# Optimization experiments

Measured on AMD Instinct MI355X. Metric: run time of the kernel, lower is better.

## Reference

```python
import jax, jax.numpy as jnp
import numpy as np

B, N, K = 32, 4096, 8          # batch, num input features (64x64 map), num slots
HID, D, DM = 256, 256, 512     # hid_dim, slot_dim, mlp_hid_dim
ITERS = 3
TEMP = 1.0
EPS = 1e-8
SCALE = D ** -0.5              # (slot_dim // num_heads) ** -0.5, heads=1


def layer_norm(x, g, b):
    m = jnp.mean(x, axis=-1, keepdims=True)
    v = jnp.mean((x - m) ** 2, axis=-1, keepdims=True)
    return (x - m) * jax.lax.rsqrt(v + 1e-5) * g + b


def setup_inputs() -> dict:
    key = jax.random.key(0)
    ks = jax.random.split(key, 20)
    s = 0.02
    inp = {
        "inputs": jax.random.normal(ks[0], (B, N, HID), jnp.float32),
        "noise": jax.random.normal(ks[1], (B, K, D), jnp.float32),
        "slots_mu": jax.random.normal(ks[2], (1, 1, D), jnp.float32),
        "slots_sigma": jnp.abs(jax.random.normal(ks[3], (1, 1, D), jnp.float32)),
        "ln_in_g": jnp.ones((HID,), jnp.float32),
        "ln_in_b": jnp.zeros((HID,), jnp.float32),
        "ln_slots_g": jnp.ones((D,), jnp.float32),
        "ln_slots_b": jnp.zeros((D,), jnp.float32),
        "ln_mlp_g": jnp.ones((D,), jnp.float32),
        "ln_mlp_b": jnp.zeros((D,), jnp.float32),
        # Linear weights stored [in, out]
        "Wq": jax.random.normal(ks[4], (D, D), jnp.float32) * s,
        "bq": jnp.zeros((D,), jnp.float32),
        "Wk": jax.random.normal(ks[5], (HID, D), jnp.float32) * s,
        "bk": jnp.zeros((D,), jnp.float32),
        "Wv": jax.random.normal(ks[6], (HID, D), jnp.float32) * s,
        "bv": jnp.zeros((D,), jnp.float32),
        # GRUCell params (torch layout transposed to [in, 3D])
        "W_ih": jax.random.normal(ks[7], (D, 3 * D), jnp.float32) * s,
        "W_hh": jax.random.normal(ks[8], (D, 3 * D), jnp.float32) * s,
        "b_ih": jnp.zeros((3 * D,), jnp.float32),
        "b_hh": jnp.zeros((3 * D,), jnp.float32),
        # residual MLP
        "W1": jax.random.normal(ks[9], (D, DM), jnp.float32) * s,
        "b1": jnp.zeros((DM,), jnp.float32),
        "W2": jax.random.normal(ks[10], (DM, D), jnp.float32) * s,
        "b2": jnp.zeros((D,), jnp.float32),
    }
    return inp


def reference(inputs, noise, slots_mu, slots_sigma,
              ln_in_g, ln_in_b, ln_slots_g, ln_slots_b, ln_mlp_g, ln_mlp_b,
              Wq, bq, Wk, bk, Wv, bv,
              W_ih, W_hh, b_ih, b_hh,
              W1, b1, W2, b2):
    x = layer_norm(inputs, ln_in_g, ln_in_b)            # [B,N,HID]
    k = x @ Wk + bk                                     # [B,N,D]
    v = x @ Wv + bv                                     # [B,N,D]

    slots = slots_mu + slots_sigma * noise              # [B,K,D]

    for _ in range(ITERS):
        slots_prev = slots
        s = layer_norm(slots, ln_slots_g, ln_slots_b)
        q = s @ Wq + bq                                  # [B,K,D]
        dots = jnp.einsum('bkd,bnd->bkn', q, k) * SCALE / TEMP
        attn = jax.nn.softmax(dots, axis=1)              # inverted: over slot axis
        attn = attn + EPS
        attn = attn / jnp.sum(attn, axis=2, keepdims=True)  # weighted mean over keys
        updates = jnp.einsum('bkn,bnd->bkd', attn, v)    # [B,K,D]

        # GRUCell on flattened (B*K, D)
        xg = updates.reshape(-1, D)
        h = slots_prev.reshape(-1, D)
        gi = xg @ W_ih + b_ih
        gh = h @ W_hh + b_hh
        i_r, i_z, i_n = jnp.split(gi, 3, axis=-1)
        h_r, h_z, h_n = jnp.split(gh, 3, axis=-1)
        r = jax.nn.sigmoid(i_r + h_r)
        z = jax.nn.sigmoid(i_z + h_z)
        n = jnp.tanh(i_n + r * h_n)
        h = (1.0 - z) * n + z * h
        slots = h.reshape(B, K, D)

        # residual MLP
        m = layer_norm(slots, ln_mlp_g, ln_mlp_b)
        slots = slots + (jax.nn.relu(m @ W1 + b1) @ W2 + b2)

    return slots
```

## Files before the change

### kernel.cpp

```cpp
#include <hip/hip_runtime.h>
#include <hip/hip_bf16.h>

#define NB 32
#define NPOS 4096
#define NSLOT 8
#define HIDD 256
#define DDIM 256
#define SCALE_F 0.0625f
#define EPS_F 1e-8f
#define NCHUNK 32
#define CPOS 128
#define TPOS 32

typedef __attribute__((ext_vector_type(4))) float f32x4;
typedef __attribute__((ext_vector_type(8))) short s16x8;
typedef __attribute__((ext_vector_type(2))) unsigned int u32x2;

__device__ __forceinline__ unsigned short f2bf(float f) {
    unsigned int x = __float_as_uint(f);
    x = (x + 0x7fffu + ((x >> 16) & 1u)) >> 16;
    return (unsigned short)x;
}
__device__ __forceinline__ float bf_lo(unsigned u) { return __uint_as_float(u << 16); }
__device__ __forceinline__ float bf_hi(unsigned u) { return __uint_as_float(u & 0xffff0000u); }

__global__ __launch_bounds__(256) void k_ln_in(
        const float* __restrict__ x, const float* __restrict__ g,
        const float* __restrict__ b, unsigned short* __restrict__ lnx) {
    int lane = threadIdx.x & 63;
    int wave = threadIdx.x >> 6;
    long row = (long)blockIdx.x * 4 + wave;
    const float4* xr = (const float4*)(x + row * 256);
    float4 v = xr[lane];
    float s = v.x + v.y + v.z + v.w;
    float sq = v.x * v.x + v.y * v.y + v.z * v.z + v.w * v.w;
    #pragma unroll
    for (int m = 32; m; m >>= 1) { s += __shfl_xor(s, m); sq += __shfl_xor(sq, m); }
    float mean = s * 0.00390625f;
    float rstd = rsqrtf(sq * 0.00390625f - mean * mean + 1e-5f);
    const float4 gg = ((const float4*)g)[lane];
    const float4 bb = ((const float4*)b)[lane];
    ushort4 o;
    o.x = f2bf((v.x - mean) * rstd * gg.x + bb.x);
    o.y = f2bf((v.y - mean) * rstd * gg.y + bb.y);
    o.z = f2bf((v.z - mean) * rstd * gg.z + bb.z);
    o.w = f2bf((v.w - mean) * rstd * gg.w + bb.w);
    ((ushort4*)(lnx + row * 256))[lane] = o;
}

__device__ __forceinline__ unsigned packrow(const float* __restrict__ W, int hp, int N, int c) {
    return (unsigned)f2bf(W[(2*hp)*N + c]) | ((unsigned)f2bf(W[(2*hp+1)*N + c]) << 16);
}

__global__ __launch_bounds__(256) void k_prep(
        const float* __restrict__ Wq, const float* __restrict__ Wk,
        const float* __restrict__ Wv, const float* __restrict__ Wih,
        const float* __restrict__ Whh, const float* __restrict__ W1,
        const float* __restrict__ W2,
        unsigned* __restrict__ WqP, unsigned* __restrict__ WkTP,
        unsigned* __restrict__ WvP, unsigned* __restrict__ WihP,
        unsigned* __restrict__ WhhP, unsigned* __restrict__ W1P,
        unsigned* __restrict__ W2P) {
    int i = blockIdx.x * 256 + threadIdx.x;
    if (i < 32768) {
        int hp = i >> 8, c = i & 255;
        WqP[i] = packrow(Wq, hp, 256, c);
        WvP[i] = packrow(Wv, hp, 256, c);
        WkTP[i] = (unsigned)f2bf(Wk[c*256 + 2*hp]) | ((unsigned)f2bf(Wk[c*256 + 2*hp + 1]) << 16);
    }
    if (i < 65536) {
        int hp1 = i >> 9, c1 = i & 511;
        W1P[i] = packrow(W1, hp1, 512, c1);
        int hp2 = i >> 8, c2 = i & 255;
        W2P[i] = packrow(W2, hp2, 256, c2);
    }
    if (i < 98304) {
        int hp = i / 768, c = i % 768;
        WihP[i] = packrow(Wih, hp, 768, c);
        WhhP[i] = packrow(Whh, hp, 768, c);
    }
}

__device__ __forceinline__ void qk_tail(
        float v0, float v1, int b, int s0,
        const float* __restrict__ lng, const float* __restrict__ lnb,
        const float* __restrict__ Wq, const float* __restrict__ bq,
        const float* __restrict__ Wk, const float* __restrict__ bk,
        unsigned short* __restrict__ qkg, float* __restrict__ qbkg,
        float (*sh)[256], float (*red)[4]) {
    int c = threadIdx.x;
    float s_0 = v0, q_0 = v0 * v0, s_1 = v1, q_1 = v1 * v1;
    #pragma unroll
    for (int m = 32; m; m >>= 1) {
        s_0 += __shfl_xor(s_0, m); q_0 += __shfl_xor(q_0, m);
        s_1 += __shfl_xor(s_1, m); q_1 += __shfl_xor(q_1, m);
    }
    if ((c & 63) == 0) { int w = c >> 6; red[w][0]=s_0; red[w][1]=q_0; red[w][2]=s_1; red[w][3]=q_1; }
    __syncthreads();
    float S0 = red[0][0]+red[1][0]+red[2][0]+red[3][0];
    float Q0 = red[0][1]+red[1][1]+red[2][1]+red[3][1];
    float S1 = red[0][2]+red[1][2]+red[2][2]+red[3][2];
    float Q1 = red[0][3]+red[1][3]+red[2][3]+red[3][3];
    float m0 = S0 * 0.00390625f, r0 = rsqrtf(Q0 * 0.00390625f - m0*m0 + 1e-5f);
    float m1 = S1 * 0.00390625f, r1 = rsqrtf(Q1 * 0.00390625f - m1*m1 + 1e-5f);
    float gc = lng[c], bc = lnb[c];
    sh[0][c] = (v0 - m0) * r0 * gc + bc;
    sh[1][c] = (v1 - m1) * r1 * gc + bc;
    __syncthreads();
    float qa0 = bq[c], qa1 = qa0;
    for (int h = 0; h < 256; h += 4) {
        float w0 = Wq[(h+0)*256+c], w1 = Wq[(h+1)*256+c];
        float w2 = Wq[(h+2)*256+c], w3 = Wq[(h+3)*256+c];
        float4 x0 = *(const float4*)&sh[0][h], x1 = *(const float4*)&sh[1][h];
        qa0 += x0.x*w0 + x0.y*w1 + x0.z*w2 + x0.w*w3;
        qa1 += x1.x*w0 + x1.y*w1 + x1.z*w2 + x1.w*w3;
    }
    __syncthreads();
    sh[0][c] = qa0; sh[1][c] = qa1;
    float bkc = bk[c];
    float p0 = qa0 * bkc, p1 = qa1 * bkc;
    #pragma unroll
    for (int m = 32; m; m >>= 1) { p0 += __shfl_xor(p0, m); p1 += __shfl_xor(p1, m); }
    __syncthreads();
    if ((c & 63) == 0) { int w = c >> 6; red[w][0] = p0; red[w][1] = p1; }
    __syncthreads();
    if (c < 2) qbkg[b*8 + s0 + c] = SCALE_F * (red[0][c]+red[1][c]+red[2][c]+red[3][c]);
    float k0 = 0.f, k1 = 0.f;
    const float* wkr = Wk + (long)c * 256;
    for (int d = 0; d < 256; d += 4) {
        float4 wk4 = *(const float4*)&wkr[d];
        float4 x0 = *(const float4*)&sh[0][d], x1 = *(const float4*)&sh[1][d];
        k0 += x0.x*wk4.x + x0.y*wk4.y + x0.z*wk4.z + x0.w*wk4.w;
        k1 += x1.x*wk4.x + x1.y*wk4.y + x1.z*wk4.z + x1.w*wk4.w;
    }
    qkg[(b*8 + s0    )*256 + c] = f2bf(SCALE_F * k0);
    qkg[(b*8 + s0 + 1)*256 + c] = f2bf(SCALE_F * k1);
}

__global__ __launch_bounds__(256) void k_init(
        const float* __restrict__ noise, const float* __restrict__ mu,
        const float* __restrict__ sig, const float* __restrict__ lng,
        const float* __restrict__ lnb, const float* __restrict__ Wq,
        const float* __restrict__ bq, const float* __restrict__ Wk,
        const float* __restrict__ bk, float* __restrict__ slots,
        unsigned short* __restrict__ qkg, float* __restrict__ qbkg) {
    __shared__ float sh[2][256];
    __shared__ float red[4][4];
    int b = blockIdx.x >> 2, rp = blockIdx.x & 3;
    int s0 = rp * 2, r0 = b * 8 + s0;
    int c = threadIdx.x;
    float v0 = mu[c] + sig[c] * noise[r0*256 + c];
    float v1 = mu[c] + sig[c] * noise[(r0+1)*256 + c];
    slots[r0*256 + c] = v0;
    slots[(r0+1)*256 + c] = v1;
    qk_tail(v0, v1, b, s0, lng, lnb, Wq, bq, Wk, bk, qkg, qbkg, sh, red);
}

__global__ __launch_bounds__(128) void k_stream(
        const unsigned short* __restrict__ lnx, const unsigned short* __restrict__ qk,
        const float* __restrict__ qbk, float* __restrict__ Upart,
        float* __restrict__ dpart) {
    __shared__ unsigned short xt[TPOS * 256];
    __shared__ float Ured[8 * 256];
    __shared__ float dred[8];
    int b = blockIdx.x >> 5, ch = blockIdx.x & 31;
    int t = threadIdx.x;
    int l = t & 63, w = t >> 6;
    for (int i = t; i < 2048; i += 128) Ured[i] = 0.f;
    if (t < 8) dred[t] = 0.f;
    int slot = l & 15, g = l >> 4;
    s16x8 qkf[8];
    float qbkv = 0.f;
    if (slot < 8) {
        const unsigned short* qrow = qk + (b*8 + slot) * 256;
        #pragma unroll
        for (int hk = 0; hk < 8; hk++)
            qkf[hk] = *(const s16x8*)(qrow + hk*32 + 8*g);
        qbkv = qbk[b*8 + slot];
    } else {
        #pragma unroll
        for (int hk = 0; hk < 8; hk++) qkf[hk] = (s16x8)0;
    }
    f32x4 uacc[16];
    #pragma unroll
    for (int i = 0; i < 16; i++) uacc[i] = (f32x4)0.f;
    float dreg = 0.f;
    int gbase = (b * NPOS + ch * CPOS) * 256;
    int pw = w * 16;
    __syncthreads();
    for (int tile = 0; tile < 4; tile++) {
        #pragma unroll
        for (int i = 0; i < 8; i++) {
            int c = t + 128 * i;
            int p = c >> 5, hc = c & 31;
            int4 v = *(const int4*)(lnx + gbase + (tile*TPOS + p)*256 + hc*8);
            *(int4*)&xt[p*256 + ((hc ^ (p & 15)) << 3)] = v;
        }
        __syncthreads();
        f32x4 acc = (f32x4)0.f;
        {
            int prow = pw + (l & 15);
            const unsigned short* xrow = &xt[prow * 256];
            int sw = prow & 15;
            #pragma unroll
            for (int hk = 0; hk < 8; hk++) {
                s16x8 a = *(const s16x8*)(xrow + (((hk*4 + g) ^ sw) << 3));
                acc = __builtin_amdgcn_mfma_f32_16x16x32_bf16(a, qkf[hk], acc, 0, 0, 0);
            }
        }
        float at[4];
        #pragma unroll
        for (int r = 0; r < 4; r++) {
            float v = acc[r] + qbkv;
            float m = v;
            m = fmaxf(m, __shfl_xor(m, 1));
            m = fmaxf(m, __shfl_xor(m, 2));
            m = fmaxf(m, __shfl_xor(m, 4));
            float e = __expf(v - m);
            float sum = e;
            sum += __shfl_xor(sum, 1);
            sum += __shfl_xor(sum, 2);
            sum += __shfl_xor(sum, 4);
            float a = e / sum;
            at[r] = a;
            dreg += a;
        }
        u32x2 a2;
        a2.x = (unsigned)f2bf(at[0]) | ((unsigned)f2bf(at[1]) << 16);
        a2.y = (unsigned)f2bf(at[2]) | ((unsigned)f2bf(at[3]) << 16);
        int p0 = pw + 4 * g;
        int hl = l & 7;
        #pragma unroll
        for (int hc = 0; hc < 16; hc++) {
            int hcol = hc * 2 + ((l & 15) >> 3);
            unsigned e0 = xt[(p0+0)*256 + ((hcol ^ ((p0+0) & 15)) << 3) + hl];
            unsigned e1 = xt[(p0+1)*256 + ((hcol ^ ((p0+1) & 15)) << 3) + hl];
            unsigned e2 = xt[(p0+2)*256 + ((hcol ^ ((p0+2) & 15)) << 3) + hl];
            unsigned e3 = xt[(p0+3)*256 + ((hcol ^ ((p0+3) & 15)) << 3) + hl];
            u32x2 b2;
            b2.x = e0 | (e1 << 16);
            b2.y = e2 | (e3 << 16);
            asm volatile("v_mfma_f32_16x16x16_bf16 %0, %1, %2, %0"
                         : "+v"(uacc[hc]) : "v"(a2), "v"(b2));
        }
        __syncthreads();
    }
    if (g < 2) {
        #pragma unroll
        for (int hc = 0; hc < 16; hc++) {
            int h = hc * 16 + (l & 15);
            #pragma unroll
            for (int r = 0; r < 4; r++)
                atomicAdd(&Ured[(4*g + r)*256 + h], uacc[hc][r]);
        }
    }
    dreg += __shfl_xor(dreg, 16);
    dreg += __shfl_xor(dreg, 32);
    if (slot < 8 && g == 0) atomicAdd(&dred[slot], dreg);
    __syncthreads();
    float* up = Upart + (long)(b * NCHUNK + ch) * 2048;
    for (int i = t; i < 2048; i += 128) up[i] = Ured[i];
    if (t < 8) dpart[(b * NCHUNK + ch) * 8 + t] = dred[t];
}

__device__ __forceinline__ float ln1024(float v, int c, const float* __restrict__ g,
                                        const float* __restrict__ b, float (*red)[2]) {
    float s1 = v, s2 = v * v;
    #pragma unroll
    for (int m = 32; m; m >>= 1) { s1 += __shfl_xor(s1, m); s2 += __shfl_xor(s2, m); }
    int w = threadIdx.x >> 6;
    if ((threadIdx.x & 63) == 0) { red[w][0] = s1; red[w][1] = s2; }
    __syncthreads();
    float S = 0.f, Q = 0.f;
    #pragma unroll
    for (int i = 0; i < 16; i++) { S += red[i][0]; Q += red[i][1]; }
    float mean = S * (1.f/1024.f);
    float rstd = rsqrtf(Q * (1.f/1024.f) - mean*mean + 1e-5f);
    __syncthreads();
    return (v - mean) * rstd * g[c] + b[c];
}

__global__ __launch_bounds__(1024) void k_post(
        const float* __restrict__ Upart, const float* __restrict__ dpart,
        const unsigned* __restrict__ WvP, const float* __restrict__ bv,
        const unsigned* __restrict__ WihP, const unsigned* __restrict__ WhhP,
        const float* __restrict__ bih, const float* __restrict__ bhh,
        const float* __restrict__ lnmg, const float* __restrict__ lnmb,
        const unsigned* __restrict__ W1P, const float* __restrict__ b1,
        const unsigned* __restrict__ W2P, const float* __restrict__ b2,
        const float* __restrict__ lnsg, const float* __restrict__ lnsb,
        const unsigned* __restrict__ WqP, const float* __restrict__ bq,
        const unsigned* __restrict__ WkTP, const float* __restrict__ bk,
        float* __restrict__ slots, unsigned short* __restrict__ qkg,
        float* __restrict__ qbkg, float* __restrict__ outp, int last) {
    __shared__ float A[256];
    __shared__ float B[256];
    __shared__ float P4[4][256];
    __shared__ float G[12][256];
    __shared__ float H2[2][512];
    __shared__ float H[512];
    __shared__ float red[16][2];
    __shared__ float scal[1];
    int r = blockIdx.x, b = r >> 3, s = r & 7;
    int t = threadIdx.x, c = t & 255, q = t >> 8;
    {
        float u = 0.f;
        const float* ub = Upart + (long)b * NCHUNK * 2048 + s * 256 + c;
        #pragma unroll
        for (int i = 0; i < 8; i++) u += ub[(q * 8 + i) * 2048];
        P4[q][c] = u;
        if (q == 1) B[c] = slots[r * 256 + c];
        if (t < 32) {
            float dv = dpart[(b * NCHUNK + t) * 8 + s];
            #pragma unroll
            for (int m = 16; m; m >>= 1) dv += __shfl_xor(dv, m);
            if (t == 0) scal[0] = dv;
        }
    }
    __syncthreads();
    float dn = 1.f / (scal[0] + (float)NPOS * EPS_F);
    if (q == 0) A[c] = P4[0][c] + P4[1][c] + P4[2][c] + P4[3][c];
    __syncthreads();
    {
        float acc = 0.f;
        const unsigned* wp = WvP + q * 32 * 256 + c;
        const float* ap = A + q * 64;
        #pragma unroll 8
        for (int i = 0; i < 32; i++) {
            unsigned wv = wp[i * 256];
            acc += ap[2*i] * bf_lo(wv) + ap[2*i+1] * bf_hi(wv);
        }
        P4[q][c] = acc;
    }
    __syncthreads();
    float updc = (P4[0][c] + P4[1][c] + P4[2][c] + P4[3][c]) * dn + bv[c];
    if (q == 0) A[c] = updc;
    __syncthreads();
    {
        const float* src = (q < 2) ? A : B;
        const unsigned* W = (q < 2) ? WihP : WhhP;
        int base = (q & 1) * 64;
        float ar = 0.f, az = 0.f, an = 0.f;
        #pragma unroll 4
        for (int i = 0; i < 64; i++) {
            int hp = base + i;
            float a0 = src[2*hp], a1 = src[2*hp+1];
            unsigned w0 = W[hp*768 + c];
            unsigned w1 = W[hp*768 + c + 256];
            unsigned w2 = W[hp*768 + c + 512];
            ar += a0*bf_lo(w0) + a1*bf_hi(w0);
            az += a0*bf_lo(w1) + a1*bf_hi(w1);
            an += a0*bf_lo(w2) + a1*bf_hi(w2);
        }
        G[q*3+0][c] = ar; G[q*3+1][c] = az; G[q*3+2][c] = an;
    }
    __syncthreads();
    float spc = B[c];
    float gir = bih[c]     + G[0][c] + G[3][c];
    float giz = bih[c+256] + G[1][c] + G[4][c];
    float gin = bih[c+512] + G[2][c] + G[5][c];
    float ghr = bhh[c]     + G[6][c] + G[9][c];
    float ghz = bhh[c+256] + G[7][c] + G[10][c];
    float ghn = bhh[c+512] + G[8][c] + G[11][c];
    float rg = 1.f/(1.f + __expf(-(gir+ghr)));
    float zg = 1.f/(1.f + __expf(-(giz+ghz)));
    float ng = tanhf(gin + rg*ghn);
    float hnew = (1.f - zg)*ng + zg*spc;
    float mmc = ln1024(hnew, c, lnmg, lnmb, red);
    if (q == 0) A[c] = mmc;
    __syncthreads();
    {
        int j = t & 511, kh = t >> 9;
        float acc = 0.f;
        #pragma unroll 8
        for (int i = 0; i < 64; i++) {
            int hp = kh*64 + i;
            unsigned wv = W1P[hp*512 + j];
            acc += A[2*hp]*bf_lo(wv) + A[2*hp+1]*bf_hi(wv);
        }
        H2[kh][j] = acc;
    }
    __syncthreads();
    if (t < 512) H[t] = fmaxf(H2[0][t] + H2[1][t] + b1[t], 0.f);
    __syncthreads();
    {
        float acc = 0.f;
        const unsigned* wp = W2P + q * 64 * 256 + c;
        const float* hb = H + q * 128;
        #pragma unroll 8
        for (int i = 0; i < 64; i++) {
            unsigned wv = wp[i * 256];
            acc += hb[2*i]*bf_lo(wv) + hb[2*i+1]*bf_hi(wv);
        }
        P4[q][c] = acc;
    }
    __syncthreads();
    float outc = hnew + P4[0][c] + P4[1][c] + P4[2][c] + P4[3][c] + b2[c];
    if (t < 256) {
        slots[r*256 + c] = outc;
        if (last) outp[r*256 + c] = outc;
    }
    if (last) return;
    float sc = ln1024(outc, c, lnsg, lnsb, red);
    if (q == 0) A[c] = sc;
    __syncthreads();
    {
        float acc = 0.f;
        const unsigned* wp = WqP + q * 32 * 256 + c;
        const float* ap = A + q * 64;
        #pragma unroll 8
        for (int i = 0; i < 32; i++) {
            unsigned wv = wp[i * 256];
            acc += ap[2*i]*bf_lo(wv) + ap[2*i+1]*bf_hi(wv);
        }
        P4[q][c] = acc;
    }
    __syncthreads();
    float qc = P4[0][c] + P4[1][c] + P4[2][c] + P4[3][c] + bq[c];
    {
        float v = qc * bk[c];
        #pragma unroll
        for (int m = 32; m; m >>= 1) v += __shfl_xor(v, m);
        int w = t >> 6;
        if ((t & 63) == 0) red[w][0] = v;
        __syncthreads();
        if (t == 0) {
            float S = 0.f;
            #pragma unroll
            for (int i = 0; i < 16; i++) S += red[i][0];
            qbkg[r] = SCALE_F * 0.25f * S;
        }
    }
    if (q == 0) A[c] = qc;
    __syncthreads();
    {
        float acc = 0.f;
        const unsigned* wp = WkTP + q * 32 * 256 + c;
        const float* ap = A + q * 64;
        #pragma unroll 8
        for (int i = 0; i < 32; i++) {
            unsigned wv = wp[i * 256];
            acc += ap[2*i]*bf_lo(wv) + ap[2*i+1]*bf_hi(wv);
        }
        P4[q][c] = acc;
    }
    __syncthreads();
    if (t < 256) qkg[r*256 + c] = f2bf(SCALE_F * (P4[0][c] + P4[1][c] + P4[2][c] + P4[3][c]));
}

extern "C" void kernel_launch(void* const* d_in, const int* in_sizes, int n_in,
                              void* d_out, int out_size, void* d_ws, size_t ws_size,
                              hipStream_t stream) {
    const float* inputs = (const float*)d_in[0];
    const float* noise  = (const float*)d_in[1];
    const float* mu     = (const float*)d_in[2];
    const float* sig    = (const float*)d_in[3];
    const float* lnig   = (const float*)d_in[4];
    const float* lnib   = (const float*)d_in[5];
    const float* lnsg   = (const float*)d_in[6];
    const float* lnsb   = (const float*)d_in[7];
    const float* lnmg   = (const float*)d_in[8];
    const float* lnmb   = (const float*)d_in[9];
    const float* Wq     = (const float*)d_in[10];
    const float* bq     = (const float*)d_in[11];
    const float* Wk     = (const float*)d_in[12];
    const float* bk     = (const float*)d_in[13];
    const float* Wv     = (const float*)d_in[14];
    const float* bv     = (const float*)d_in[15];
    const float* Wih    = (const float*)d_in[16];
    const float* Whh    = (const float*)d_in[17];
    const float* bih    = (const float*)d_in[18];
    const float* bhh    = (const float*)d_in[19];
    const float* W1     = (const float*)d_in[20];
    const float* b1     = (const float*)d_in[21];
    const float* W2     = (const float*)d_in[22];
    const float* b2     = (const float*)d_in[23];

    char* ws = (char*)d_ws;
    unsigned short* lnx = (unsigned short*)ws;
    size_t off = (size_t)NB * NPOS * HIDD * 2;
    unsigned short* qkb = (unsigned short*)(ws + off); off += (size_t)NB*NSLOT*HIDD*2;
    float* qbk   = (float*)(ws + off); off += (size_t)NB*NSLOT*4;
    float* Upart = (float*)(ws + off); off += (size_t)NB*NCHUNK*NSLOT*HIDD*4;
    float* dpart = (float*)(ws + off); off += (size_t)NB*NCHUNK*NSLOT*4;
    float* slots = (float*)(ws + off); off += (size_t)NB*NSLOT*DDIM*4;
    unsigned* WqP  = (unsigned*)(ws + off); off += 32768u*4;
    unsigned* WkTP = (unsigned*)(ws + off); off += 32768u*4;
    unsigned* WvP  = (unsigned*)(ws + off); off += 32768u*4;
    unsigned* WihP = (unsigned*)(ws + off); off += 98304u*4;
    unsigned* WhhP = (unsigned*)(ws + off); off += 98304u*4;
    unsigned* W1P  = (unsigned*)(ws + off); off += 65536u*4;
    unsigned* W2P  = (unsigned*)(ws + off); off += 65536u*4;

    k_prep<<<384, 256, 0, stream>>>(Wq, Wk, Wv, Wih, Whh, W1, W2,
                                    WqP, WkTP, WvP, WihP, WhhP, W1P, W2P);
    k_ln_in<<<NB*NPOS/4, 256, 0, stream>>>(inputs, lnig, lnib, lnx);
    k_init<<<NB*4, 256, 0, stream>>>(noise, mu, sig, lnsg, lnsb, Wq, bq, Wk, bk,
                                     slots, qkb, qbk);
    for (int it = 0; it < 3; it++) {
        k_stream<<<NB*NCHUNK, 128, 0, stream>>>(lnx, qkb, qbk, Upart, dpart);
        k_post<<<NB*NSLOT, 1024, 0, stream>>>(Upart, dpart,
                                              WvP, bv, WihP, WhhP, bih, bhh,
                                              lnmg, lnmb, W1P, b1, W2P, b2,
                                              lnsg, lnsb, WqP, bq, WkTP, bk,
                                              slots, qkb, qbk, (float*)d_out,
                                              it == 2 ? 1 : 0);
    }
}
```

Baseline: 242.9 us.

## Split post-processing into per-batch kernels, precompute Wq·Wkᵀ, use fp16 dot2

The monolithic per-slot k_post kernel is replaced by a chain of smaller kernels: reduce, value projection, GRU, two MLP stages, and a query/key kernel. Each of these processes all 8 slots of a batch, so every weight load is reused across 8 rows. The query and key projections are folded algebraically into one precomputed matrix M1 = Wq·Wkᵀ plus bias vectors, which removes one GEMV per iteration. Packed weights move from bf16 to fp16 and use the hardware fdot2 instruction. The cost is about six extra kernel launches per iteration, extra global round-trips for intermediates, and a change in the rounding of the precomputed fused matrix and of fp16 activations.

```diff
diff --git a/kernel.cpp b/kernel.cpp
--- a/kernel.cpp
+++ b/kernel.cpp
@@ -15,14 +15,54 @@
 typedef __attribute__((ext_vector_type(4))) float f32x4;
 typedef __attribute__((ext_vector_type(8))) short s16x8;
 typedef __attribute__((ext_vector_type(2))) unsigned int u32x2;
+typedef _Float16 h16x2 __attribute__((ext_vector_type(2)));
 
 __device__ __forceinline__ unsigned short f2bf(float f) {
     unsigned int x = __float_as_uint(f);
     x = (x + 0x7fffu + ((x >> 16) & 1u)) >> 16;
     return (unsigned short)x;
 }
-__device__ __forceinline__ float bf_lo(unsigned u) { return __uint_as_float(u << 16); }
-__device__ __forceinline__ float bf_hi(unsigned u) { return __uint_as_float(u & 0xffff0000u); }
+__device__ __forceinline__ unsigned short f2h(float f) {
+    _Float16 h = (_Float16)f;
+    return __builtin_bit_cast(unsigned short, h);
+}
+__device__ __forceinline__ h16x2 u2h(unsigned u) { return __builtin_bit_cast(h16x2, u); }
+__device__ __forceinline__ h16x2 mkh(float a0, float a1) {
+    h16x2 r; r[0] = (_Float16)a0; r[1] = (_Float16)a1; return r;
+}
+
+__device__ __forceinline__ float blkred(float v, float* red4) {
+    #pragma unroll
+    for (int m = 32; m; m >>= 1) v += __shfl_xor(v, m);
+    int w = threadIdx.x >> 6;
+    if ((threadIdx.x & 63) == 0) red4[w] = v;
+    __syncthreads();
+    float s = red4[0] + red4[1] + red4[2] + red4[3];
+    __syncthreads();
+    return s;
+}
+
+__device__ __forceinline__ void ln8rows(float (*sl)[256], const float* __restrict__ g,
+                                        const float* __restrict__ b) {
+    int lane = threadIdx.x & 63, wv = threadIdx.x >> 6;
+    #pragma unroll
+    for (int rr = 0; rr < 2; rr++) {
+        int s = wv * 2 + rr;
+        float ss = 0.f, sq = 0.f;
+        #pragma unroll
+        for (int j = 0; j < 4; j++) { float v = sl[s][lane*4+j]; ss += v; sq += v*v; }
+        #pragma unroll
+        for (int m = 32; m; m >>= 1) { ss += __shfl_xor(ss, m); sq += __shfl_xor(sq, m); }
+        float mean = ss * 0.00390625f;
+        float rstd = rsqrtf(sq * 0.00390625f - mean*mean + 1e-5f);
+        #pragma unroll
+        for (int j = 0; j < 4; j++) {
+            int d = lane*4 + j;
+            sl[s][d] = (sl[s][d] - mean) * rstd * g[d] + b[d];
+        }
+    }
+    __syncthreads();
+}
 
 __global__ __launch_bounds__(256) void k_ln_in(
         const float* __restrict__ x, const float* __restrict__ g,
@@ -48,112 +88,102 @@
     ((ushort4*)(lnx + row * 256))[lane] = o;
 }
 
-__device__ __forceinline__ unsigned packrow(const float* __restrict__ W, int hp, int N, int c) {
-    return (unsigned)f2bf(W[(2*hp)*N + c]) | ((unsigned)f2bf(W[(2*hp+1)*N + c]) << 16);
+__device__ __forceinline__ unsigned packrowh(const float* __restrict__ W, int hp, int N, int c) {
+    return (unsigned)f2h(W[(2*hp)*N + c]) | ((unsigned)f2h(W[(2*hp+1)*N + c]) << 16);
 }
 
 __global__ __launch_bounds__(256) void k_prep(
-        const float* __restrict__ Wq, const float* __restrict__ Wk,
         const float* __restrict__ Wv, const float* __restrict__ Wih,
         const float* __restrict__ Whh, const float* __restrict__ W1,
         const float* __restrict__ W2,
-        unsigned* __restrict__ WqP, unsigned* __restrict__ WkTP,
         unsigned* __restrict__ WvP, unsigned* __restrict__ WihP,
         unsigned* __restrict__ WhhP, unsigned* __restrict__ W1P,
         unsigned* __restrict__ W2P) {
     int i = blockIdx.x * 256 + threadIdx.x;
     if (i < 32768) {
         int hp = i >> 8, c = i & 255;
-        WqP[i] = packrow(Wq, hp, 256, c);
-        WvP[i] = packrow(Wv, hp, 256, c);
-        WkTP[i] = (unsigned)f2bf(Wk[c*256 + 2*hp]) | ((unsigned)f2bf(Wk[c*256 + 2*hp + 1]) << 16);
+        WvP[i] = packrowh(Wv, hp, 256, c);
     }
     if (i < 65536) {
         int hp1 = i >> 9, c1 = i & 511;
-        W1P[i] = packrow(W1, hp1, 512, c1);
+        W1P[i] = packrowh(W1, hp1, 512, c1);
         int hp2 = i >> 8, c2 = i & 255;
-        W2P[i] = packrow(W2, hp2, 256, c2);
+        W2P[i] = packrowh(W2, hp2, 256, c2);
     }
     if (i < 98304) {
         int hp = i / 768, c = i % 768;
-        WihP[i] = packrow(Wih, hp, 768, c);
-        WhhP[i] = packrow(Whh, hp, 768, c);
-    }
-}
-
-__device__ __forceinline__ void qk_tail(
-        float v0, float v1, int b, int s0,
-        const float* __restrict__ lng, const float* __restrict__ lnb,
-        const float* __restrict__ Wq, const float* __restrict__ bq,
-        const float* __restrict__ Wk, const float* __restrict__ bk,
-        unsigned short* __restrict__ qkg, float* __restrict__ qbkg,
-        float (*sh)[256], float (*red)[4]) {
-    int c = threadIdx.x;
-    float s_0 = v0, q_0 = v0 * v0, s_1 = v1, q_1 = v1 * v1;
-    #pragma unroll
-    for (int m = 32; m; m >>= 1) {
-        s_0 += __shfl_xor(s_0, m); q_0 += __shfl_xor(q_0, m);
-        s_1 += __shfl_xor(s_1, m); q_1 += __shfl_xor(q_1, m);
-    }
-    if ((c & 63) == 0) { int w = c >> 6; red[w][0]=s_0; red[w][1]=q_0; red[w][2]=s_1; red[w][3]=q_1; }
-    __syncthreads();
-    float S0 = red[0][0]+red[1][0]+red[2][0]+red[3][0];
-    float Q0 = red[0][1]+red[1][1]+red[2][1]+red[3][1];
-    float S1 = red[0][2]+red[1][2]+red[2][2]+red[3][2];
-    float Q1 = red[0][3]+red[1][3]+red[2][3]+red[3][3];
-    float m0 = S0 * 0.00390625f, r0 = rsqrtf(Q0 * 0.00390625f - m0*m0 + 1e-5f);
-    float m1 = S1 * 0.00390625f, r1 = rsqrtf(Q1 * 0.00390625f - m1*m1 + 1e-5f);
-    float gc = lng[c], bc = lnb[c];
-    sh[0][c] = (v0 - m0) * r0 * gc + bc;
-    sh[1][c] = (v1 - m1) * r1 * gc + bc;
-    __syncthreads();
-    float qa0 = bq[c], qa1 = qa0;
-    for (int h = 0; h < 256; h += 4) {
-        float w0 = Wq[(h+0)*256+c], w1 = Wq[(h+1)*256+c];
-        float w2 = Wq[(h+2)*256+c], w3 = Wq[(h+3)*256+c];
-        float4 x0 = *(const float4*)&sh[0][h], x1 = *(const float4*)&sh[1][h];
-        qa0 += x0.x*w0 + x0.y*w1 + x0.z*w2 + x0.w*w3;
-        qa1 += x1.x*w0 + x1.y*w1 + x1.z*w2 + x1.w*w3;
-    }
-    __syncthreads();
-    sh[0][c] = qa0; sh[1][c] = qa1;
-    float bkc = bk[c];
-    float p0 = qa0 * bkc, p1 = qa1 * bkc;
-    #pragma unroll
-    for (int m = 32; m; m >>= 1) { p0 += __shfl_xor(p0, m); p1 += __shfl_xor(p1, m); }
-    __syncthreads();
-    if ((c & 63) == 0) { int w = c >> 6; red[w][0] = p0; red[w][1] = p1; }
-    __syncthreads();
-    if (c < 2) qbkg[b*8 + s0 + c] = SCALE_F * (red[0][c]+red[1][c]+red[2][c]+red[3][c]);
-    float k0 = 0.f, k1 = 0.f;
-    const float* wkr = Wk + (long)c * 256;
-    for (int d = 0; d < 256; d += 4) {
-        float4 wk4 = *(const float4*)&wkr[d];
-        float4 x0 = *(const float4*)&sh[0][d], x1 = *(const float4*)&sh[1][d];
-        k0 += x0.x*wk4.x + x0.y*wk4.y + x0.z*wk4.z + x0.w*wk4.w;
-        k1 += x1.x*wk4.x + x1.y*wk4.y + x1.z*wk4.z + x1.w*wk4.w;
-    }
-    qkg[(b*8 + s0    )*256 + c] = f2bf(SCALE_F * k0);
-    qkg[(b*8 + s0 + 1)*256 + c] = f2bf(SCALE_F * k1);
-}
-
-__global__ __launch_bounds__(256) void k_init(
+        WihP[i] = packrowh(Wih, hp, 768, c);
+        WhhP[i] = packrowh(Whh, hp, 768, c);
+    }
+}
+
+__global__ __launch_bounds__(256) void k_fuse(
+        const float* __restrict__ Wq, const float* __restrict__ Wk,
+        const float* __restrict__ bq, const float* __restrict__ bk,
+        float* __restrict__ M1, float* __restrict__ v1,
+        float* __restrict__ w2, float* __restrict__ sc2) {
+    __shared__ float wq[256], bqL[256];
+    __shared__ float red4[4];
+    int e = blockIdx.x, t = threadIdx.x;
+    wq[t] = Wq[e*256 + t];
+    bqL[t] = bq[t];
+    __syncthreads();
+    const float4* wkr = (const float4*)(Wk + (long)t * 256);
+    float acc = 0.f;
+    for (int d = 0; d < 64; d++) {
+        float4 k4 = wkr[d];
+        acc += wq[4*d]*k4.x + wq[4*d+1]*k4.y + wq[4*d+2]*k4.z + wq[4*d+3]*k4.w;
+    }
+    M1[e*256 + t] = acc;
+    float p = blkred(wq[t] * bk[t], red4);
+    if (t == 0) w2[e] = p;
+    if (e == 0) {
+        float a2 = 0.f;
+        for (int d = 0; d < 64; d++) {
+            float4 k4 = wkr[d];
+            a2 += bqL[4*d]*k4.x + bqL[4*d+1]*k4.y + bqL[4*d+2]*k4.z + bqL[4*d+3]*k4.w;
+        }
+        v1[t] = a2;
+        float p2 = blkred(bqL[t] * bk[t], red4);
+        if (t == 0) sc2[0] = p2;
+    }
+}
+
+__global__ __launch_bounds__(256) void k_init2(
         const float* __restrict__ noise, const float* __restrict__ mu,
-        const float* __restrict__ sig, const float* __restrict__ lng,
-        const float* __restrict__ lnb, const float* __restrict__ Wq,
-        const float* __restrict__ bq, const float* __restrict__ Wk,
-        const float* __restrict__ bk, float* __restrict__ slots,
-        unsigned short* __restrict__ qkg, float* __restrict__ qbkg) {
-    __shared__ float sh[2][256];
-    __shared__ float red[4][4];
-    int b = blockIdx.x >> 2, rp = blockIdx.x & 3;
-    int s0 = rp * 2, r0 = b * 8 + s0;
-    int c = threadIdx.x;
-    float v0 = mu[c] + sig[c] * noise[r0*256 + c];
-    float v1 = mu[c] + sig[c] * noise[(r0+1)*256 + c];
-    slots[r0*256 + c] = v0;
-    slots[(r0+1)*256 + c] = v1;
-    qk_tail(v0, v1, b, s0, lng, lnb, Wq, bq, Wk, bk, qkg, qbkg, sh, red);
+        const float* __restrict__ sig, float* __restrict__ slots) {
+    int i = blockIdx.x * 256 + threadIdx.x;
+    int c = i & 255;
+    slots[i] = mu[c] + sig[c] * noise[i];
+}
+
+__global__ __launch_bounds__(256) void S_qk(
+        const float* __restrict__ slots, const float* __restrict__ lng,
+        const float* __restrict__ lnb, const float* __restrict__ M1,
+        const float* __restrict__ v1, const float* __restrict__ w2,
+        const float* __restrict__ sc2, unsigned short* __restrict__ qkg,
+        float* __restrict__ qbkg) {
+    __shared__ float sl[8][256];
+    __shared__ float red4[4];
+    int b = blockIdx.x >> 3, cg = blockIdx.x & 7;
+    int t = threadIdx.x;
+    #pragma unroll
+    for (int s = 0; s < 8; s++) sl[s][t] = slots[(b*8+s)*256 + t];
+    __syncthreads();
+    ln8rows(sl, lng, lnb);
+    if (cg == 0) {
+        float w2t = w2[t], sc2v = sc2[0];
+        #pragma unroll
+        for (int s = 0; s < 8; s++) {
+            float p = blkred(sl[s][t] * w2t, red4);
+            if (t == 0) qbkg[b*8+s] = SCALE_F * (p + sc2v);
+        }
+    }
+    int s = t >> 5, j = t & 31, c = cg*32 + j;
+    float acc = v1[c];
+    #pragma unroll 8
+    for (int d = 0; d < 256; d++) acc += sl[s][d] * M1[d*256 + c];
+    qkg[(b*8+s)*256 + c] = f2bf(SCALE_F * acc);
 }
 
 __global__ __launch_bounds__(128) void k_stream(
@@ -263,189 +293,121 @@
     if (t < 8) dpart[(b * NCHUNK + ch) * 8 + t] = dred[t];
 }
 
-__device__ __forceinline__ float ln1024(float v, int c, const float* __restrict__ g,
-                                        const float* __restrict__ b, float (*red)[2]) {
-    float s1 = v, s2 = v * v;
-    #pragma unroll
-    for (int m = 32; m; m >>= 1) { s1 += __shfl_xor(s1, m); s2 += __shfl_xor(s2, m); }
-    int w = threadIdx.x >> 6;
-    if ((threadIdx.x & 63) == 0) { red[w][0] = s1; red[w][1] = s2; }
-    __syncthreads();
-    float S = 0.f, Q = 0.f;
-    #pragma unroll
-    for (int i = 0; i < 16; i++) { S += red[i][0]; Q += red[i][1]; }
-    float mean = S * (1.f/1024.f);
-    float rstd = rsqrtf(Q * (1.f/1024.f) - mean*mean + 1e-5f);
-    __syncthreads();
-    return (v - mean) * rstd * g[c] + b[c];
-}
-
-__global__ __launch_bounds__(1024) void k_post(
+__global__ __launch_bounds__(256) void S_red(
         const float* __restrict__ Upart, const float* __restrict__ dpart,
+        float* __restrict__ U, float* __restrict__ den) {
+    int b = blockIdx.x, t = threadIdx.x;
+    const float* ub = Upart + (long)b * NCHUNK * 2048;
+    for (int i = t; i < 2048; i += 256) {
+        float s = 0.f;
+        #pragma unroll 8
+        for (int ch = 0; ch < NCHUNK; ch++) s += ub[ch*2048 + i];
+        U[b*2048 + i] = s;
+    }
+    if (t < 8) {
+        float s = 0.f;
+        for (int ch = 0; ch < NCHUNK; ch++) s += dpart[(b*NCHUNK + ch)*8 + t];
+        den[b*8 + t] = s;
+    }
+}
+
+__global__ __launch_bounds__(256) void S_upd(
+        const float* __restrict__ U, const float* __restrict__ den,
         const unsigned* __restrict__ WvP, const float* __restrict__ bv,
+        float* __restrict__ updates) {
+    __shared__ float U8[8][256];
+    __shared__ float dnl[8];
+    int b = blockIdx.x >> 3, cg = blockIdx.x & 7;
+    int t = threadIdx.x;
+    #pragma unroll
+    for (int s = 0; s < 8; s++) U8[s][t] = U[(b*8+s)*256 + t];
+    if (t < 8) dnl[t] = 1.f / (den[b*8+t] + (float)NPOS * EPS_F);
+    __syncthreads();
+    int s = t >> 5, j = t & 31, c = cg*32 + j;
+    float acc = 0.f;
+    #pragma unroll 8
+    for (int dp = 0; dp < 128; dp++)
+        acc = __builtin_amdgcn_fdot2(mkh(U8[s][2*dp], U8[s][2*dp+1]),
+                                     u2h(WvP[dp*256 + c]), acc, false);
+    updates[(b*8+s)*256 + c] = acc * dnl[s] + bv[c];
+}
+
+__global__ __launch_bounds__(256) void S_gru(
+        const float* __restrict__ updates, const float* __restrict__ slots,
         const unsigned* __restrict__ WihP, const unsigned* __restrict__ WhhP,
         const float* __restrict__ bih, const float* __restrict__ bhh,
-        const float* __restrict__ lnmg, const float* __restrict__ lnmb,
-        const unsigned* __restrict__ W1P, const float* __restrict__ b1,
-        const unsigned* __restrict__ W2P, const float* __restrict__ b2,
-        const float* __restrict__ lnsg, const float* __restrict__ lnsb,
-        const unsigned* __restrict__ WqP, const float* __restrict__ bq,
-        const unsigned* __restrict__ WkTP, const float* __restrict__ bk,
-        float* __restrict__ slots, unsigned short* __restrict__ qkg,
-        float* __restrict__ qbkg, float* __restrict__ outp, int last) {
-    __shared__ float A[256];
-    __shared__ float B[256];
-    __shared__ float P4[4][256];
-    __shared__ float G[12][256];
-    __shared__ float H2[2][512];
-    __shared__ float H[512];
-    __shared__ float red[16][2];
-    __shared__ float scal[1];
-    int r = blockIdx.x, b = r >> 3, s = r & 7;
-    int t = threadIdx.x, c = t & 255, q = t >> 8;
-    {
-        float u = 0.f;
-        const float* ub = Upart + (long)b * NCHUNK * 2048 + s * 256 + c;
-        #pragma unroll
-        for (int i = 0; i < 8; i++) u += ub[(q * 8 + i) * 2048];
-        P4[q][c] = u;
-        if (q == 1) B[c] = slots[r * 256 + c];
-        if (t < 32) {
-            float dv = dpart[(b * NCHUNK + t) * 8 + s];
-            #pragma unroll
-            for (int m = 16; m; m >>= 1) dv += __shfl_xor(dv, m);
-            if (t == 0) scal[0] = dv;
-        }
-    }
-    __syncthreads();
-    float dn = 1.f / (scal[0] + (float)NPOS * EPS_F);
-    if (q == 0) A[c] = P4[0][c] + P4[1][c] + P4[2][c] + P4[3][c];
-    __syncthreads();
-    {
-        float acc = 0.f;
-        const unsigned* wp = WvP + q * 32 * 256 + c;
-        const float* ap = A + q * 64;
-        #pragma unroll 8
-        for (int i = 0; i < 32; i++) {
-            unsigned wv = wp[i * 256];
-            acc += ap[2*i] * bf_lo(wv) + ap[2*i+1] * bf_hi(wv);
-        }
-        P4[q][c] = acc;
-    }
-    __syncthreads();
-    float updc = (P4[0][c] + P4[1][c] + P4[2][c] + P4[3][c]) * dn + bv[c];
-    if (q == 0) A[c] = updc;
-    __syncthreads();
-    {
-        const float* src = (q < 2) ? A : B;
-        const unsigned* W = (q < 2) ? WihP : WhhP;
-        int base = (q & 1) * 64;
-        float ar = 0.f, az = 0.f, an = 0.f;
-        #pragma unroll 4
-        for (int i = 0; i < 64; i++) {
-            int hp = base + i;
-            float a0 = src[2*hp], a1 = src[2*hp+1];
-            unsigned w0 = W[hp*768 + c];
-            unsigned w1 = W[hp*768 + c + 256];
-            unsigned w2 = W[hp*768 + c + 512];
-            ar += a0*bf_lo(w0) + a1*bf_hi(w0);
-            az += a0*bf_lo(w1) + a1*bf_hi(w1);
-            an += a0*bf_lo(w2) + a1*bf_hi(w2);
-        }
-        G[q*3+0][c] = ar; G[q*3+1][c] = az; G[q*3+2][c] = an;
-    }
-    __syncthreads();
-    float spc = B[c];
-    float gir = bih[c]     + G[0][c] + G[3][c];
-    float giz = bih[c+256] + G[1][c] + G[4][c];
-    float gin = bih[c+512] + G[2][c] + G[5][c];
-    float ghr = bhh[c]     + G[6][c] + G[9][c];
-    float ghz = bhh[c+256] + G[7][c] + G[10][c];
-    float ghn = bhh[c+512] + G[8][c] + G[11][c];
+        float* __restrict__ hnewg) {
+    __shared__ float uL[8][256], sL[8][256];
+    int b = blockIdx.x >> 3, cg = blockIdx.x & 7;
+    int t = threadIdx.x;
+    #pragma unroll
+    for (int s = 0; s < 8; s++) {
+        uL[s][t] = updates[(b*8+s)*256 + t];
+        sL[s][t] = slots[(b*8+s)*256 + t];
+    }
+    __syncthreads();
+    int s = t >> 5, j = t & 31, c = cg*32 + j;
+    float gir = bih[c], giz = bih[c+256], gin = bih[c+512];
+    float ghr = bhh[c], ghz = bhh[c+256], ghn = bhh[c+512];
+    #pragma unroll 4
+    for (int dp = 0; dp < 128; dp++) {
+        h16x2 au = mkh(uL[s][2*dp], uL[s][2*dp+1]);
+        h16x2 as_ = mkh(sL[s][2*dp], sL[s][2*dp+1]);
+        gir = __builtin_amdgcn_fdot2(au, u2h(WihP[dp*768 + c]),       gir, false);
+        giz = __builtin_amdgcn_fdot2(au, u2h(WihP[dp*768 + c + 256]), giz, false);
+        gin = __builtin_amdgcn_fdot2(au, u2h(WihP[dp*768 + c + 512]), gin, false);
+        ghr = __builtin_amdgcn_fdot2(as_, u2h(WhhP[dp*768 + c]),       ghr, false);
+        ghz = __builtin_amdgcn_fdot2(as_, u2h(WhhP[dp*768 + c + 256]), ghz, false);
+        ghn = __builtin_amdgcn_fdot2(as_, u2h(WhhP[dp*768 + c + 512]), ghn, false);
+    }
     float rg = 1.f/(1.f + __expf(-(gir+ghr)));
     float zg = 1.f/(1.f + __expf(-(giz+ghz)));
     float ng = tanhf(gin + rg*ghn);
-    float hnew = (1.f - zg)*ng + zg*spc;
-    float mmc = ln1024(hnew, c, lnmg, lnmb, red);
-    if (q == 0) A[c] = mmc;
-    __syncthreads();
-    {
-        int j = t & 511, kh = t >> 9;
-        float acc = 0.f;
-        #pragma unroll 8
-        for (int i = 0; i < 64; i++) {
-            int hp = kh*64 + i;
-            unsigned wv = W1P[hp*512 + j];
-            acc += A[2*hp]*bf_lo(wv) + A[2*hp+1]*bf_hi(wv);
-        }
-        H2[kh][j] = acc;
-    }
-    __syncthreads();
-    if (t < 512) H[t] = fmaxf(H2[0][t] + H2[1][t] + b1[t], 0.f);
-    __syncthreads();
-    {
-        float acc = 0.f;
-        const unsigned* wp = W2P + q * 64 * 256 + c;
-        const float* hb = H + q * 128;
-        #pragma unroll 8
-        for (int i = 0; i < 64; i++) {
-            unsigned wv = wp[i * 256];
-            acc += hb[2*i]*bf_lo(wv) + hb[2*i+1]*bf_hi(wv);
-        }
-        P4[q][c] = acc;
-    }
-    __syncthreads();
-    float outc = hnew + P4[0][c] + P4[1][c] + P4[2][c] + P4[3][c] + b2[c];
-    if (t < 256) {
-        slots[r*256 + c] = outc;
-        if (last) outp[r*256 + c] = outc;
-    }
-    if (last) return;
-    float sc = ln1024(outc, c, lnsg, lnsb, red);
-    if (q == 0) A[c] = sc;
-    __syncthreads();
-    {
-        float acc = 0.f;
-        const unsigned* wp = WqP + q * 32 * 256 + c;
-        const float* ap = A + q * 64;
-        #pragma unroll 8
-        for (int i = 0; i < 32; i++) {
-            unsigned wv = wp[i * 256];
-            acc += ap[2*i]*bf_lo(wv) + ap[2*i+1]*bf_hi(wv);
-        }
-        P4[q][c] = acc;
-    }
-    __syncthreads();
-    float qc = P4[0][c] + P4[1][c] + P4[2][c] + P4[3][c] + bq[c];
-    {
-        float v = qc * bk[c];
-        #pragma unroll
-        for (int m = 32; m; m >>= 1) v += __shfl_xor(v, m);
-        int w = t >> 6;
-        if ((t & 63) == 0) red[w][0] = v;
-        __syncthreads();
-        if (t == 0) {
-            float S = 0.f;
-            #pragma unroll
-            for (int i = 0; i < 16; i++) S += red[i][0];
-            qbkg[r] = SCALE_F * 0.25f * S;
-        }
-    }
-    if (q == 0) A[c] = qc;
-    __syncthreads();
-    {
-        float acc = 0.f;
-        const unsigned* wp = WkTP + q * 32 * 256 + c;
-        const float* ap = A + q * 64;
-        #pragma unroll 8
-        for (int i = 0; i < 32; i++) {
-            unsigned wv = wp[i * 256];
-            acc += ap[2*i]*bf_lo(wv) + ap[2*i+1]*bf_hi(wv);
-        }
-        P4[q][c] = acc;
-    }
-    __syncthreads();
-    if (t < 256) qkg[r*256 + c] = f2bf(SCALE_F * (P4[0][c] + P4[1][c] + P4[2][c] + P4[3][c]));
+    hnewg[(b*8+s)*256 + c] = (1.f - zg)*ng + zg*sL[s][c];
+}
+
+__global__ __launch_bounds__(256) void S_mlp1(
+        const float* __restrict__ hnewg, const float* __restrict__ lng,
+        const float* __restrict__ lnb, const unsigned* __restrict__ W1P,
+        const float* __restrict__ b1, float* __restrict__ Hbuf) {
+    __shared__ float hn[8][256];
+    int b = blockIdx.x >> 3, cg = blockIdx.x & 7;
+    int t = threadIdx.x;
+    #pragma unroll
+    for (int s = 0; s < 8; s++) hn[s][t] = hnewg[(b*8+s)*256 + t];
+    __syncthreads();
+    ln8rows(hn, lng, lnb);
+    int s = t >> 5, j = t & 31;
+    int j0 = cg*64 + j;
+    float a0 = b1[j0], a1 = b1[j0 + 32];
+    #pragma unroll 4
+    for (int dp = 0; dp < 128; dp++) {
+        h16x2 av = mkh(hn[s][2*dp], hn[s][2*dp+1]);
+        a0 = __builtin_amdgcn_fdot2(av, u2h(W1P[dp*512 + j0]),      a0, false);
+        a1 = __builtin_amdgcn_fdot2(av, u2h(W1P[dp*512 + j0 + 32]), a1, false);
+    }
+    Hbuf[(b*8+s)*512 + j0]      = fmaxf(a0, 0.f);
+    Hbuf[(b*8+s)*512 + j0 + 32] = fmaxf(a1, 0.f);
+}
+
+__global__ __launch_bounds__(256) void S_mlp2(
+        const float* __restrict__ Hbuf, const float* __restrict__ hnewg,
+        const unsigned* __restrict__ W2P, const float* __restrict__ b2,
+        float* __restrict__ slots, float* __restrict__ outp, int last) {
+    __shared__ float Hl[8][512];
+    int b = blockIdx.x >> 3, cg = blockIdx.x & 7;
+    int t = threadIdx.x;
+    for (int i = t; i < 4096; i += 256) Hl[i >> 9][i & 511] = Hbuf[(long)b*4096 + i];
+    __syncthreads();
+    int s = t >> 5, j = t & 31, c = cg*32 + j;
+    float acc = 0.f;
+    #pragma unroll 8
+    for (int hp = 0; hp < 256; hp++)
+        acc = __builtin_amdgcn_fdot2(mkh(Hl[s][2*hp], Hl[s][2*hp+1]),
+                                     u2h(W2P[hp*256 + c]), acc, false);
+    float outv = hnewg[(b*8+s)*256 + c] + acc + b2[c];
+    slots[(b*8+s)*256 + c] = outv;
+    if (last) outp[(b*8+s)*256 + c] = outv;
 }
 
 extern "C" void kernel_launch(void* const* d_in, const int* in_sizes, int n_in,
@@ -484,26 +446,33 @@
     float* Upart = (float*)(ws + off); off += (size_t)NB*NCHUNK*NSLOT*HIDD*4;
     float* dpart = (float*)(ws + off); off += (size_t)NB*NCHUNK*NSLOT*4;
     float* slots = (float*)(ws + off); off += (size_t)NB*NSLOT*DDIM*4;
-    unsigned* WqP  = (unsigned*)(ws + off); off += 32768u*4;
-    unsigned* WkTP = (unsigned*)(ws + off); off += 32768u*4;
     unsigned* WvP  = (unsigned*)(ws + off); off += 32768u*4;
     unsigned* WihP = (unsigned*)(ws + off); off += 98304u*4;
     unsigned* WhhP = (unsigned*)(ws + off); off += 98304u*4;
     unsigned* W1P  = (unsigned*)(ws + off); off += 65536u*4;
     unsigned* W2P  = (unsigned*)(ws + off); off += 65536u*4;
-
-    k_prep<<<384, 256, 0, stream>>>(Wq, Wk, Wv, Wih, Whh, W1, W2,
-                                    WqP, WkTP, WvP, WihP, WhhP, W1P, W2P);
+    float* M1   = (float*)(ws + off); off += 65536u*4;
+    float* v1   = (float*)(ws + off); off += 256*4;
+    float* w2   = (float*)(ws + off); off += 256*4;
+    float* sc2  = (float*)(ws + off); off += 64;
+    float* U    = (float*)(ws + off); off += (size_t)NB*NSLOT*DDIM*4;
+    float* den  = (float*)(ws + off); off += (size_t)NB*NSLOT*4;
+    float* upd  = (float*)(ws + off); off += (size_t)NB*NSLOT*DDIM*4;
+    float* hng  = (float*)(ws + off); off += (size_t)NB*NSLOT*DDIM*4;
+    float* Hbuf = (float*)(ws + off); off += (size_t)NB*NSLOT*512*4;
+
+    k_prep<<<384, 256, 0, stream>>>(Wv, Wih, Whh, W1, W2, WvP, WihP, WhhP, W1P, W2P);
+    k_fuse<<<256, 256, 0, stream>>>(Wq, Wk, bq, bk, M1, v1, w2, sc2);
     k_ln_in<<<NB*NPOS/4, 256, 0, stream>>>(inputs, lnig, lnib, lnx);
-    k_init<<<NB*4, 256, 0, stream>>>(noise, mu, sig, lnsg, lnsb, Wq, bq, Wk, bk,
-                                     slots, qkb, qbk);
+    k_init2<<<256, 256, 0, stream>>>(noise, mu, sig, slots);
     for (int it = 0; it < 3; it++) {
+        S_qk<<<NB*8, 256, 0, stream>>>(slots, lnsg, lnsb, M1, v1, w2, sc2, qkb, qbk);
         k_stream<<<NB*NCHUNK, 128, 0, stream>>>(lnx, qkb, qbk, Upart, dpart);
-        k_post<<<NB*NSLOT, 1024, 0, stream>>>(Upart, dpart,
-                                              WvP, bv, WihP, WhhP, bih, bhh,
-                                              lnmg, lnmb, W1P, b1, W2P, b2,
-                                              lnsg, lnsb, WqP, bq, WkTP, bk,
-                                              slots, qkb, qbk, (float*)d_out,
-                                              it == 2 ? 1 : 0);
-    }
-}
+        S_red<<<NB, 256, 0, stream>>>(Upart, dpart, U, den);
+        S_upd<<<NB*8, 256, 0, stream>>>(U, den, WvP, bv, upd);
+        S_gru<<<NB*8, 256, 0, stream>>>(upd, slots, WihP, WhhP, bih, bhh, hng);
+        S_mlp1<<<NB*8, 256, 0, stream>>>(hng, lnmg, lnmb, W1P, b1, Hbuf);
+        S_mlp2<<<NB*8, 256, 0, stream>>>(Hbuf, hng, W2P, b2, slots, (float*)d_out,
+                                         it == 2 ? 1 : 0);
+    }
+}
```

Measured after the change: 402.3 us. +65.6%, slower.
